# Optimization experiments

Measured on AMD Instinct MI355X. Metric: run time of the kernel, lower is better.

The kernel has to match this reference:

```python
import jax, jax.numpy as jnp
import numpy as np

D_MODEL = 768
N_HEADS = 4
N_POINTS = 4
PATCH = 16
IMG = 224
HF = IMG // PATCH  # 14
WF = IMG // PATCH  # 14
LQ = HF * WF       # 196 tokens
DH = D_MODEL // N_HEADS  # 192


def setup_inputs() -> dict:
    key = jax.random.key(0)
    ks = jax.random.split(key, 14)
    s = 0.02
    inp = {
        "x": jax.random.normal(ks[0], (4, 16, 3, IMG, IMG), dtype=jnp.float32),
        # patch-embed conv (Conv2d 3->768, k=16, s=16)
        "embed_w": s * jax.random.normal(ks[1], (D_MODEL, 3, PATCH, PATCH), dtype=jnp.float32),
        "embed_b": jnp.zeros((D_MODEL,), dtype=jnp.float32),
        # MSDeformAttn linears (nn.Linear stores W as [out, in]; y = x @ W.T + b)
        "value_w": s * jax.random.normal(ks[2], (D_MODEL, D_MODEL), dtype=jnp.float32),
        "value_b": jnp.zeros((D_MODEL,), dtype=jnp.float32),
        "off_w": s * jax.random.normal(ks[3], (N_HEADS * N_POINTS * 2, D_MODEL), dtype=jnp.float32),
        "off_b": s * jax.random.normal(ks[4], (N_HEADS * N_POINTS * 2,), dtype=jnp.float32),
        "aw_w": s * jax.random.normal(ks[5], (N_HEADS * N_POINTS, D_MODEL), dtype=jnp.float32),
        "aw_b": jnp.zeros((N_HEADS * N_POINTS,), dtype=jnp.float32),
        "outp_w": s * jax.random.normal(ks[6], (D_MODEL, D_MODEL), dtype=jnp.float32),
        "outp_b": jnp.zeros((D_MODEL,), dtype=jnp.float32),
        # final nn.Linear proj
        "proj_w": s * jax.random.normal(ks[7], (D_MODEL, D_MODEL), dtype=jnp.float32),
        "proj_b": jnp.zeros((D_MODEL,), dtype=jnp.float32),
    }
    return inp


def _patch_embed(x, w, b):
    # x: (N,3,H,W); non-overlapping 16x16 patches == Conv2d(3,D,16,16)
    N = x.shape[0]
    xh = x.reshape(N, 3, HF, PATCH, WF, PATCH)
    feat = jnp.einsum('nchpwq,dcpq->nhwd', xh, w) + b  # (N,HF,WF,D)
    return feat.reshape(N, LQ, D_MODEL)


def _ref_points():
    lin = jnp.linspace(0.0, 1.0, HF)
    gy, gx = jnp.meshgrid(lin, lin, indexing='ij')
    return jnp.stack([gx, gy], -1).reshape(LQ, 2)  # (Lq, 2) in [0,1], (x,y)


def _deform_attn_core(value, loc, attn):
    # value: (N, Lq, M, Dh); loc: (N, Lq, M, P, 2) normalized [0,1]; attn: (N, Lq, M, P)
    N = value.shape[0]
    # grid_sample align_corners=False: pixel = (2*loc-1 + 1)*S/2 - 0.5 = loc*S - 0.5
    px = loc[..., 0] * WF - 0.5
    py = loc[..., 1] * HF - 0.5
    x0 = jnp.floor(px).astype(jnp.int32)
    y0 = jnp.floor(py).astype(jnp.int32)
    x1, y1 = x0 + 1, y0 + 1
    wx1 = px - x0.astype(px.dtype)
    wy1 = py - y0.astype(py.dtype)
    wx0, wy0 = 1.0 - wx1, 1.0 - wy1

    valh = value.transpose(0, 2, 1, 3)  # (N, M, HW, Dh)

    def gather(ix, iy):
        valid = (ix >= 0) & (ix < WF) & (iy >= 0) & (iy < HF)  # zeros padding
        idx = jnp.clip(iy, 0, HF - 1) * WF + jnp.clip(ix, 0, WF - 1)
        idxm = idx.transpose(0, 2, 1, 3).reshape(N, N_HEADS, LQ * N_POINTS)
        g = jnp.take_along_axis(valh, idxm[..., None], axis=2)  # (N,M,Lq*P,Dh)
        g = g * valid.transpose(0, 2, 1, 3).reshape(N, N_HEADS, LQ * N_POINTS, 1)
        return g.reshape(N, N_HEADS, LQ, N_POINTS, DH)

    def w4(a, b):  # (N,Lq,M,P) -> (N,M,Lq,P,1)
        return (a * b).transpose(0, 2, 1, 3)[..., None]

    sampled = (w4(wx0, wy0) * gather(x0, y0) + w4(wx1, wy0) * gather(x1, y0)
               + w4(wx0, wy1) * gather(x0, y1) + w4(wx1, wy1) * gather(x1, y1))
    # weighted combine over points
    out = (sampled * attn.transpose(0, 2, 1, 3)[..., None]).sum(3)  # (N,M,Lq,Dh)
    return out.transpose(0, 2, 1, 3).reshape(N, LQ, D_MODEL)


def reference(x, embed_w, embed_b, value_w, value_b, off_w, off_b, aw_w, aw_b,
              outp_w, outp_b, proj_w, proj_b):
    B, T = x.shape[0], x.shape[1]
    N = B * T
    xi = x.reshape(N, 3, IMG, IMG)
    feat = _patch_embed(xi, embed_w, embed_b)  # (N, Lq, D)

    # MSDeformAttn (n_levels=1)
    value = (feat @ value_w.T + value_b).reshape(N, LQ, N_HEADS, DH)
    off = (feat @ off_w.T + off_b).reshape(N, LQ, N_HEADS, N_POINTS, 2)
    aw = (feat @ aw_w.T + aw_b).reshape(N, LQ, N_HEADS, N_POINTS)
    aw = jax.nn.softmax(aw, axis=-1)  # softmax over n_levels*n_points = 4

    ref = _ref_points()  # (Lq, 2)
    norm = jnp.array([WF, HF], dtype=feat.dtype)  # offset_normalizer = (W, H)
    loc = ref[None, :, None, None, :] + off / norm  # (N,Lq,M,P,2)

    out = _deform_attn_core(value, loc, aw)
    out = out @ outp_w.T + outp_b  # output_proj

    pooled = out.mean(axis=1)  # mean over tokens
    final = pooled @ proj_w.T + proj_b
    return final.reshape(B, T, D_MODEL)
```

## Files before the change

### kernel.cpp

```cpp
#include <hip/hip_runtime.h>
#include <hip/hip_bf16.h>


using bf16 = __bf16;
typedef bf16  bf16x8 __attribute__((ext_vector_type(8)));
typedef float f32x4  __attribute__((ext_vector_type(4)));

#define N_IMG   64
#define LQ      196
#define DM      768
#define NH      4
#define DH      192
#define M_ROWS  (N_IMG * LQ)
#define NCAT    896

#define B_WGEMM   0
#define B_BCAT    42
#define B_ZERO    46
#define B_IM2COL  94
#define STAGE_GRID (B_IM2COL + 9408)

#define OFF_A     ((size_t)0)
#define OFF_WC    (OFF_A    + 19267584)
#define OFF_BCAT  (OFF_WC   + 1376256)
#define OFF_VBUF  (OFF_BCAT + 4096)
#define OFF_OA    (OFF_VBUF + 19267584)
#define OFF_CORE  (OFF_OA   + 3211264)
#define OFF_POOL  (OFF_CORE + 196608)

__device__ __forceinline__ void gload_lds16(const bf16* g, bf16* l) {
#if __has_builtin(__builtin_amdgcn_global_load_lds)
  __builtin_amdgcn_global_load_lds(
      (const __attribute__((address_space(1))) void*)g,
      (__attribute__((address_space(3))) void*)l, 16, 0, 0);
#else
  *(bf16x8*)l = *(const bf16x8*)g;
#endif
}

__global__ void stage_kernel(const float* __restrict__ x,
                             const float* __restrict__ embed_w,
                             const float* __restrict__ embed_b,
                             const float* __restrict__ value_w,
                             const float* __restrict__ off_w,
                             const float* __restrict__ aw_w,
                             const float* __restrict__ value_b,
                             const float* __restrict__ off_b,
                             const float* __restrict__ aw_b,
                             bf16* __restrict__ A,
                             bf16* __restrict__ Wc,
                             float* __restrict__ bcat2,
                             float* __restrict__ core) {
  __shared__ bf16 As[128 * 64];
  __shared__ bf16 Bs[128 * 64];
  const int bid = blockIdx.x;
  const int tid = threadIdx.x;

  if (bid >= B_IM2COL) {
    const int t   = (bid - B_IM2COL) * 256 + tid;
    const int row = t / 192;
    const int j   = t - row * 192;
    const int k   = j * 4;
    const int c   = k >> 8;
    const int r   = k & 255;
    const int p   = r >> 4;
    const int q   = r & 15;
    const int n   = row / 196;
    const int lq  = row - n * 196;
    const int h   = lq / 14;
    const int w   = lq - h * 14;
    const float4 v = *(const float4*)(x +
        ((((size_t)n * 3 + c) * 224) + h * 16 + p) * 224 + w * 16 + q);
    bf16* dst = A + (size_t)row * DM + k;
    dst[0] = (bf16)v.x; dst[1] = (bf16)v.y; dst[2] = (bf16)v.z; dst[3] = (bf16)v.w;
    return;
  }

  if (bid < B_BCAT) {
    const int mT = bid / 6;
    const int nT = bid - mT * 6;
    const int oBase = mT * 128;
    const int nBase = nT * 128;
    const int wave = tid >> 6;
    const int lane = tid & 63;
    const int quad = lane >> 4;
    const int r16  = lane & 15;
    const int wm = wave & 1;
    const int wn = wave >> 1;
    const int srow = wave * 32 + (lane >> 3);
    const int scol = (lane & 7) * 8;

    const float* asrc[4];
#pragma unroll
    for (int i = 0; i < 4; ++i) {
      const int o = oBase + srow + i * 8;
      asrc[i] = (o < 768) ? value_w + (size_t)o * DM
              : (o < 800) ? off_w + (size_t)(o - 768) * DM
              : (o < 816) ? aw_w + (size_t)(o - 800) * DM : nullptr;
    }

    const f32x4 zero = {0.f, 0.f, 0.f, 0.f};
    f32x4 acc[4][4];
#pragma unroll
    for (int mi = 0; mi < 4; ++mi)
#pragma unroll
      for (int ni = 0; ni < 4; ++ni) acc[mi][ni] = zero;

    for (int kt = 0; kt < DM; kt += 64) {
#pragma unroll
      for (int i = 0; i < 4; ++i) {
        const int r = srow + i * 8;
        bf16x8 av;
        if (asrc[i]) {
          const float4 f0 = *(const float4*)(asrc[i] + kt + scol);
          const float4 f1 = *(const float4*)(asrc[i] + kt + scol + 4);
          av[0] = (bf16)f0.x; av[1] = (bf16)f0.y;
          av[2] = (bf16)f0.z; av[3] = (bf16)f0.w;
          av[4] = (bf16)f1.x; av[5] = (bf16)f1.y;
          av[6] = (bf16)f1.z; av[7] = (bf16)f1.w;
        } else {
#pragma unroll
          for (int jj = 0; jj < 8; ++jj) av[jj] = (bf16)0.f;
        }
        *(bf16x8*)&As[r * 64 + scol] = av;
        const int n = nBase + r;
        bf16x8 bv;
#pragma unroll
        for (int jj = 0; jj < 8; ++jj)
          bv[jj] = (bf16)embed_w[(size_t)(kt + scol + jj) * DM + n];
        *(bf16x8*)&Bs[r * 64 + scol] = bv;
      }
      __syncthreads();
#pragma unroll
      for (int kk = 0; kk < 64; kk += 32) {
        bf16x8 af[4], bfr[4];
#pragma unroll
        for (int mi = 0; mi < 4; ++mi)
          af[mi] = *(const bf16x8*)&As[(wm * 64 + mi * 16 + r16) * 64 + kk + quad * 8];
#pragma unroll
        for (int ni = 0; ni < 4; ++ni)
          bfr[ni] = *(const bf16x8*)&Bs[(wn * 64 + ni * 16 + r16) * 64 + kk + quad * 8];
#pragma unroll
        for (int mi = 0; mi < 4; ++mi)
#pragma unroll
          for (int ni = 0; ni < 4; ++ni)
            acc[mi][ni] = __builtin_amdgcn_mfma_f32_16x16x32_bf16(
                af[mi], bfr[ni], acc[mi][ni], 0, 0, 0);
      }
      __syncthreads();
    }
#pragma unroll
    for (int ni = 0; ni < 4; ++ni) {
      const int col = nBase + wn * 64 + ni * 16 + r16;
#pragma unroll
      for (int mi = 0; mi < 4; ++mi) {
        const int row0 = oBase + wm * 64 + mi * 16 + quad * 4;
#pragma unroll
        for (int rr = 0; rr < 4; ++rr)
          Wc[(size_t)(row0 + rr) * DM + col] = (bf16)acc[mi][ni][rr];
      }
    }
    return;
  }

  if (bid < B_ZERO) {
    const int o = (bid - B_BCAT) * 256 + tid;
    if (o < NCAT) {
      float bias_o = (o < 768) ? value_b[o]
                   : (o < 800) ? off_b[o - 768]
                   : (o < 816) ? aw_b[o - 800] : 0.f;
      float acc = 0.f;
      if (o < 816) {
        const float* wr = (o < 768) ? value_w + (size_t)o * DM
                        : (o < 800) ? off_w + (size_t)(o - 768) * DM
                        : aw_w + (size_t)(o - 800) * DM;
        const float4* w4p = (const float4*)wr;
        const float4* b4p = (const float4*)embed_b;
#pragma unroll 4
        for (int k = 0; k < DM / 4; ++k) {
          const float4 wv = w4p[k], bv = b4p[k];
          acc += wv.x * bv.x + wv.y * bv.y + wv.z * bv.z + wv.w * bv.w;
        }
      }
      bcat2[o] = acc + bias_o;
    }
    return;
  }

  const int i = (bid - B_ZERO) * 256 + tid;
  f32x4 z = {0.f, 0.f, 0.f, 0.f};
  ((f32x4*)core)[i] = z;
}

__global__ void gemm2_mixed(const bf16* __restrict__ A, const bf16* __restrict__ B,
                            const float* __restrict__ bias,
                            bf16* __restrict__ Vb, float* __restrict__ OA,
                            int M, int N, int K) {
  __shared__ bf16 As[128 * 64];
  __shared__ bf16 Bs[128 * 64];

  const int tid  = threadIdx.x;
  const int wave = tid >> 6;
  const int lane = tid & 63;
  const int nBase = blockIdx.x * 128;
  const int mBase = blockIdx.y * 128;
  const int wm = wave & 1;
  const int wn = wave >> 1;
  const int quad = lane >> 4;
  const int r16  = lane & 15;

  const f32x4 zero = {0.f, 0.f, 0.f, 0.f};
  f32x4 acc[4][4];
#pragma unroll
  for (int mi = 0; mi < 4; ++mi)
#pragma unroll
    for (int ni = 0; ni < 4; ++ni) acc[mi][ni] = zero;

  const int srow = wave * 32 + (lane >> 3);
  const int scol = (lane & 7) * 8;
  const bf16* Ag = A + (size_t)(mBase + srow) * K + scol;
  const bf16* Bg = B + (size_t)(nBase + srow) * K + scol;
  bf16* Al = As + srow * 64 + scol;
  bf16* Bl = Bs + srow * 64 + scol;

  for (int kt = 0; kt < K; kt += 64) {
#pragma unroll
    for (int i = 0; i < 4; ++i) {
      gload_lds16(Ag + (size_t)(i * 8) * K + kt, Al + i * 8 * 64);
      gload_lds16(Bg + (size_t)(i * 8) * K + kt, Bl + i * 8 * 64);
    }
    __syncthreads();
#pragma unroll
    for (int kk = 0; kk < 64; kk += 32) {
      bf16x8 af[4], bfr[4];
#pragma unroll
      for (int mi = 0; mi < 4; ++mi)
        af[mi] = *(const bf16x8*)&As[(wm * 64 + mi * 16 + r16) * 64 + kk + quad * 8];
#pragma unroll
      for (int ni = 0; ni < 4; ++ni)
        bfr[ni] = *(const bf16x8*)&Bs[(wn * 64 + ni * 16 + r16) * 64 + kk + quad * 8];
#pragma unroll
      for (int mi = 0; mi < 4; ++mi)
#pragma unroll
        for (int ni = 0; ni < 4; ++ni)
          acc[mi][ni] = __builtin_amdgcn_mfma_f32_16x16x32_bf16(
              af[mi], bfr[ni], acc[mi][ni], 0, 0, 0);
    }
    __syncthreads();
  }

#pragma unroll
  for (int ni = 0; ni < 4; ++ni) {
    const int col = nBase + wn * 64 + ni * 16 + r16;
    const float bv = bias[col];
#pragma unroll
    for (int mi = 0; mi < 4; ++mi) {
      const int row0 = mBase + wm * 64 + mi * 16 + quad * 4;
#pragma unroll
      for (int rr = 0; rr < 4; ++rr) {
        float v = acc[mi][ni][rr] + bv;
        int row = row0 + rr;
        if (col < 768) {
          Vb[(size_t)row * 768 + col] = (bf16)v;
        } else if (col < 816) {
          OA[(size_t)row * 64 + (col - 768)] = v;
        }
      }
    }
  }
}

__global__ void deform_kernel(const bf16* __restrict__ Vb,
                              const float* __restrict__ OA,
                              float* __restrict__ core) {
  __shared__ float s_w[64][4];
  __shared__ int   s_t[64][4];

  const int n   = blockIdx.x;
  const int lq0 = blockIdx.y * 4;
  const int z   = blockIdx.z;
  const int tid = threadIdx.x;

  if (tid < 64) {
    const int i = tid >> 4;
    const int m = (tid >> 2) & 3;
    const int p = tid & 3;
    const int lq = lq0 + i;
    const float* row = OA + ((size_t)n * LQ + lq) * 64;

    const float l0 = row[32 + m * 4 + 0];
    const float l1 = row[32 + m * 4 + 1];
    const float l2 = row[32 + m * 4 + 2];
    const float l3 = row[32 + m * 4 + 3];
    const float mx = fmaxf(fmaxf(l0, l1), fmaxf(l2, l3));
    const float e0 = __expf(l0 - mx), e1 = __expf(l1 - mx);
    const float e2 = __expf(l2 - mx), e3 = __expf(l3 - mx);
    const float inv = 1.f / (e0 + e1 + e2 + e3);
    const float ep[4] = {e0, e1, e2, e3};
    const float ew = ep[p] * inv;

    const int h = lq / 14, w = lq - (lq / 14) * 14;
    const float px = (float)w * (14.f / 13.f) - 0.5f + row[(m * 4 + p) * 2 + 0];
    const float py = (float)h * (14.f / 13.f) - 0.5f + row[(m * 4 + p) * 2 + 1];
    const float fx = floorf(px), fy = floorf(py);
    const int x0 = (int)fx, y0 = (int)fy;
    const float wx1 = px - fx, wy1 = py - fy;
    const float wx0 = 1.f - wx1, wy0 = 1.f - wy1;

    const bool vx0 = (x0 >= 0) & (x0 < 14);
    const bool vx1 = (x0 >= -1) & (x0 < 13);
    const bool vy0 = (y0 >= 0) & (y0 < 14);
    const bool vy1 = (y0 >= -1) & (y0 < 13);
    const int cx0 = min(max(x0, 0), 13),      cx1 = min(max(x0 + 1, 0), 13);
    const int cy0 = min(max(y0, 0), 13) * 14, cy1 = min(max(y0 + 1, 0), 13) * 14;

    s_w[tid][0] = (vx0 & vy0) ? ew * wx0 * wy0 : 0.f;
    s_w[tid][1] = (vx1 & vy0) ? ew * wx1 * wy0 : 0.f;
    s_w[tid][2] = (vx0 & vy1) ? ew * wx0 * wy1 : 0.f;
    s_w[tid][3] = (vx1 & vy1) ? ew * wx1 * wy1 : 0.f;
    s_t[tid][0] = cy0 + cx0;
    s_t[tid][1] = cy0 + cx1;
    s_t[tid][2] = cy1 + cx0;
    s_t[tid][3] = cy1 + cx1;
  }
  __syncthreads();

  const int ch = z * 256 + tid;
  const int m  = ch / DH;
  const bf16* vb = Vb + (size_t)n * LQ * 768 + ch;
  float acc = 0.f;
#pragma unroll
  for (int i = 0; i < 4; ++i) {
#pragma unroll
    for (int p = 0; p < 4; ++p) {
      const int e = i * 16 + m * 4 + p;
      const float4 w4 = *(const float4*)s_w[e];
      const int4   t4 = *(const int4*)s_t[e];
      acc += w4.x * (float)vb[(size_t)t4.x * 768];
      acc += w4.y * (float)vb[(size_t)t4.y * 768];
      acc += w4.z * (float)vb[(size_t)t4.z * 768];
      acc += w4.w * (float)vb[(size_t)t4.w * 768];
    }
  }
  atomicAdd(&core[(size_t)n * DM + ch], acc * (1.f / 196.f));
}

__global__ void small_linear4(const float* __restrict__ in,
                              const float* __restrict__ W,
                              const float* __restrict__ b,
                              float* __restrict__ out) {
  __shared__ float s_in[4 * DM];
  const int tid = threadIdx.x;
  const int n0 = blockIdx.x * 4;
  const float4* src = (const float4*)(in + (size_t)n0 * DM);
#pragma unroll
  for (int i = 0; i < 3; ++i)
    ((float4*)s_in)[tid + i * 256] = src[tid + i * 256];
  __syncthreads();

  const int d = blockIdx.y * 256 + tid;
  const float4* w4p = (const float4*)(W + (size_t)d * DM);
  const float4* s0 = (const float4*)(s_in);
  const float4* s1 = (const float4*)(s_in + DM);
  const float4* s2 = (const float4*)(s_in + 2 * DM);
  const float4* s3 = (const float4*)(s_in + 3 * DM);
  float a0 = 0.f, a1 = 0.f, a2 = 0.f, a3 = 0.f;
#pragma unroll 4
  for (int k = 0; k < DM / 4; ++k) {
    const float4 w = w4p[k];
    const float4 v0 = s0[k], v1 = s1[k], v2 = s2[k], v3 = s3[k];
    a0 += w.x * v0.x + w.y * v0.y + w.z * v0.z + w.w * v0.w;
    a1 += w.x * v1.x + w.y * v1.y + w.z * v1.z + w.w * v1.w;
    a2 += w.x * v2.x + w.y * v2.y + w.z * v2.z + w.w * v2.w;
    a3 += w.x * v3.x + w.y * v3.y + w.z * v3.z + w.w * v3.w;
  }
  const float bv = b[d];
  out[(size_t)(n0 + 0) * DM + d] = a0 + bv;
  out[(size_t)(n0 + 1) * DM + d] = a1 + bv;
  out[(size_t)(n0 + 2) * DM + d] = a2 + bv;
  out[(size_t)(n0 + 3) * DM + d] = a3 + bv;
}

extern "C" void kernel_launch(void* const* d_in, const int* in_sizes, int n_in,
                              void* d_out, int out_size, void* d_ws, size_t ws_size,
                              hipStream_t stream) {
  const float* x       = (const float*)d_in[0];
  const float* embed_w = (const float*)d_in[1];
  const float* embed_b = (const float*)d_in[2];
  const float* value_w = (const float*)d_in[3];
  const float* value_b = (const float*)d_in[4];
  const float* off_w   = (const float*)d_in[5];
  const float* off_b   = (const float*)d_in[6];
  const float* aw_w    = (const float*)d_in[7];
  const float* aw_b    = (const float*)d_in[8];
  const float* outp_w  = (const float*)d_in[9];
  const float* outp_b  = (const float*)d_in[10];
  const float* proj_w  = (const float*)d_in[11];
  const float* proj_b  = (const float*)d_in[12];
  float* out = (float*)d_out;

  char* ws = (char*)d_ws;
  bf16*  A      = (bf16*)(ws + OFF_A);
  bf16*  Wc     = (bf16*)(ws + OFF_WC);
  float* bcat2  = (float*)(ws + OFF_BCAT);
  bf16*  Vbuf   = (bf16*)(ws + OFF_VBUF);
  float* OA     = (float*)(ws + OFF_OA);
  float* core   = (float*)(ws + OFF_CORE);
  float* pooled = (float*)(ws + OFF_POOL);

  stage_kernel<<<dim3(STAGE_GRID), dim3(256), 0, stream>>>(
      x, embed_w, embed_b, value_w, off_w, aw_w, value_b, off_b, aw_b,
      A, Wc, bcat2, core);

  gemm2_mixed<<<dim3(NCAT / 128, M_ROWS / 128), dim3(256), 0, stream>>>(
      A, Wc, bcat2, Vbuf, OA, M_ROWS, NCAT, DM);

  deform_kernel<<<dim3(N_IMG, 49, 3), dim3(256), 0, stream>>>(Vbuf, OA, core);

  small_linear4<<<dim3(N_IMG / 4, 3), dim3(256), 0, stream>>>(core, outp_w, outp_b, pooled);
  small_linear4<<<dim3(N_IMG / 4, 3), dim3(256), 0, stream>>>(pooled, proj_w, proj_b, out);
}
```

Baseline: 279.7 us.

## Split weight prep into separate kernel with pre-transposed bf16 weights for fold GEMM

A new prep kernel converts the concatenated value/offset/attention weights to bf16 and writes a transposed bf16 copy of the patch-embed weight. The weight-folding GEMM then reads these directly from global memory into MFMA fragments, without LDS staging or the strided fp32 loads it did before. The im2col store is also vectorised to 4-wide bf16 writes. This adds a kernel launch and extra workspace traffic in exchange for a cheaper fold GEMM that no longer holds up the long stage kernel.

Result: slower. 287.7 us (+2.9%).

```diff
diff --git a/kernel.cpp b/kernel.cpp
--- a/kernel.cpp
+++ b/kernel.cpp
@@ -3,6 +3,7 @@
 
 
 using bf16 = __bf16;
+typedef bf16  bf16x4 __attribute__((ext_vector_type(4)));
 typedef bf16  bf16x8 __attribute__((ext_vector_type(8)));
 typedef float f32x4  __attribute__((ext_vector_type(4)));
 
@@ -14,19 +15,25 @@
 #define M_ROWS  (N_IMG * LQ)
 #define NCAT    896
 
+#define P_WET    0
+#define P_WCAT   288
+#define P_BCAT   624
+#define P_ZERO   628
+#define PREP_GRID 676
+
 #define B_WGEMM   0
-#define B_BCAT    42
-#define B_ZERO    46
-#define B_IM2COL  94
+#define B_IM2COL  42
 #define STAGE_GRID (B_IM2COL + 9408)
 
 #define OFF_A     ((size_t)0)
-#define OFF_WC    (OFF_A    + 19267584)
-#define OFF_BCAT  (OFF_WC   + 1376256)
-#define OFF_VBUF  (OFF_BCAT + 4096)
-#define OFF_OA    (OFF_VBUF + 19267584)
-#define OFF_CORE  (OFF_OA   + 3211264)
-#define OFF_POOL  (OFF_CORE + 196608)
+#define OFF_WC    (OFF_A     + 19267584)
+#define OFF_BCAT  (OFF_WC    + 1376256)
+#define OFF_VBUF  (OFF_BCAT  + 4096)
+#define OFF_OA    (OFF_VBUF  + 19267584)
+#define OFF_CORE  (OFF_OA    + 3211264)
+#define OFF_POOL  (OFF_CORE  + 196608)
+#define OFF_WCATB (OFF_POOL  + 196608)
+#define OFF_WET   (OFF_WCATB + 1376256)
 
 __device__ __forceinline__ void gload_lds16(const bf16* g, bf16* l) {
 #if __has_builtin(__builtin_amdgcn_global_load_lds)
@@ -38,133 +45,56 @@
 #endif
 }
 
-__global__ void stage_kernel(const float* __restrict__ x,
-                             const float* __restrict__ embed_w,
-                             const float* __restrict__ embed_b,
-                             const float* __restrict__ value_w,
-                             const float* __restrict__ off_w,
-                             const float* __restrict__ aw_w,
-                             const float* __restrict__ value_b,
-                             const float* __restrict__ off_b,
-                             const float* __restrict__ aw_b,
-                             bf16* __restrict__ A,
-                             bf16* __restrict__ Wc,
-                             float* __restrict__ bcat2,
-                             float* __restrict__ core) {
-  __shared__ bf16 As[128 * 64];
-  __shared__ bf16 Bs[128 * 64];
+__global__ void prep_kernel(const float* __restrict__ embed_w,
+                            const float* __restrict__ embed_b,
+                            const float* __restrict__ value_w,
+                            const float* __restrict__ off_w,
+                            const float* __restrict__ aw_w,
+                            const float* __restrict__ value_b,
+                            const float* __restrict__ off_b,
+                            const float* __restrict__ aw_b,
+                            bf16* __restrict__ WeT,
+                            bf16* __restrict__ Wcatb,
+                            float* __restrict__ bcat2,
+                            float* __restrict__ core) {
   const int bid = blockIdx.x;
   const int tid = threadIdx.x;
 
-  if (bid >= B_IM2COL) {
-    const int t   = (bid - B_IM2COL) * 256 + tid;
-    const int row = t / 192;
-    const int j   = t - row * 192;
-    const int k   = j * 4;
-    const int c   = k >> 8;
-    const int r   = k & 255;
-    const int p   = r >> 4;
-    const int q   = r & 15;
-    const int n   = row / 196;
-    const int lq  = row - n * 196;
-    const int h   = lq / 14;
-    const int w   = lq - h * 14;
-    const float4 v = *(const float4*)(x +
-        ((((size_t)n * 3 + c) * 224) + h * 16 + p) * 224 + w * 16 + q);
-    bf16* dst = A + (size_t)row * DM + k;
-    dst[0] = (bf16)v.x; dst[1] = (bf16)v.y; dst[2] = (bf16)v.z; dst[3] = (bf16)v.w;
+  if (bid < P_WCAT) {
+    const int t = bid * 256 + tid;
+    const int e = t / 96;
+    const int g = t - e * 96;
+    bf16x8 o;
+#pragma unroll
+    for (int j = 0; j < 8; ++j)
+      o[j] = (bf16)embed_w[(size_t)(g * 8 + j) * DM + e];
+    *(bf16x8*)(WeT + (size_t)e * DM + g * 8) = o;
     return;
   }
 
-  if (bid < B_BCAT) {
-    const int mT = bid / 6;
-    const int nT = bid - mT * 6;
-    const int oBase = mT * 128;
-    const int nBase = nT * 128;
-    const int wave = tid >> 6;
-    const int lane = tid & 63;
-    const int quad = lane >> 4;
-    const int r16  = lane & 15;
-    const int wm = wave & 1;
-    const int wn = wave >> 1;
-    const int srow = wave * 32 + (lane >> 3);
-    const int scol = (lane & 7) * 8;
-
-    const float* asrc[4];
-#pragma unroll
-    for (int i = 0; i < 4; ++i) {
-      const int o = oBase + srow + i * 8;
-      asrc[i] = (o < 768) ? value_w + (size_t)o * DM
-              : (o < 800) ? off_w + (size_t)(o - 768) * DM
-              : (o < 816) ? aw_w + (size_t)(o - 800) * DM : nullptr;
-    }
-
-    const f32x4 zero = {0.f, 0.f, 0.f, 0.f};
-    f32x4 acc[4][4];
-#pragma unroll
-    for (int mi = 0; mi < 4; ++mi)
-#pragma unroll
-      for (int ni = 0; ni < 4; ++ni) acc[mi][ni] = zero;
-
-    for (int kt = 0; kt < DM; kt += 64) {
-#pragma unroll
-      for (int i = 0; i < 4; ++i) {
-        const int r = srow + i * 8;
-        bf16x8 av;
-        if (asrc[i]) {
-          const float4 f0 = *(const float4*)(asrc[i] + kt + scol);
-          const float4 f1 = *(const float4*)(asrc[i] + kt + scol + 4);
-          av[0] = (bf16)f0.x; av[1] = (bf16)f0.y;
-          av[2] = (bf16)f0.z; av[3] = (bf16)f0.w;
-          av[4] = (bf16)f1.x; av[5] = (bf16)f1.y;
-          av[6] = (bf16)f1.z; av[7] = (bf16)f1.w;
-        } else {
-#pragma unroll
-          for (int jj = 0; jj < 8; ++jj) av[jj] = (bf16)0.f;
-        }
-        *(bf16x8*)&As[r * 64 + scol] = av;
-        const int n = nBase + r;
-        bf16x8 bv;
-#pragma unroll
-        for (int jj = 0; jj < 8; ++jj)
-          bv[jj] = (bf16)embed_w[(size_t)(kt + scol + jj) * DM + n];
-        *(bf16x8*)&Bs[r * 64 + scol] = bv;
-      }
-      __syncthreads();
-#pragma unroll
-      for (int kk = 0; kk < 64; kk += 32) {
-        bf16x8 af[4], bfr[4];
-#pragma unroll
-        for (int mi = 0; mi < 4; ++mi)
-          af[mi] = *(const bf16x8*)&As[(wm * 64 + mi * 16 + r16) * 64 + kk + quad * 8];
-#pragma unroll
-        for (int ni = 0; ni < 4; ++ni)
-          bfr[ni] = *(const bf16x8*)&Bs[(wn * 64 + ni * 16 + r16) * 64 + kk + quad * 8];
-#pragma unroll
-        for (int mi = 0; mi < 4; ++mi)
-#pragma unroll
-          for (int ni = 0; ni < 4; ++ni)
-            acc[mi][ni] = __builtin_amdgcn_mfma_f32_16x16x32_bf16(
-                af[mi], bfr[ni], acc[mi][ni], 0, 0, 0);
-      }
-      __syncthreads();
-    }
-#pragma unroll
-    for (int ni = 0; ni < 4; ++ni) {
-      const int col = nBase + wn * 64 + ni * 16 + r16;
-#pragma unroll
-      for (int mi = 0; mi < 4; ++mi) {
-        const int row0 = oBase + wm * 64 + mi * 16 + quad * 4;
-#pragma unroll
-        for (int rr = 0; rr < 4; ++rr)
-          Wc[(size_t)(row0 + rr) * DM + col] = (bf16)acc[mi][ni][rr];
-      }
-    }
+  if (bid < P_BCAT) {
+    const int t = (bid - P_WCAT) * 256 + tid;
+    const int rr = t / 96;
+    const int g  = t - rr * 96;
+    const float* src = (rr < 768) ? value_w + (size_t)rr * DM
+                     : (rr < 800) ? off_w + (size_t)(rr - 768) * DM
+                     : (rr < 816) ? aw_w + (size_t)(rr - 800) * DM : nullptr;
+    bf16x8 o;
+    if (src) {
+      const float4 f0 = *(const float4*)(src + g * 8);
+      const float4 f1 = *(const float4*)(src + g * 8 + 4);
+      o[0] = (bf16)f0.x; o[1] = (bf16)f0.y; o[2] = (bf16)f0.z; o[3] = (bf16)f0.w;
+      o[4] = (bf16)f1.x; o[5] = (bf16)f1.y; o[6] = (bf16)f1.z; o[7] = (bf16)f1.w;
+    } else {
+#pragma unroll
+      for (int j = 0; j < 8; ++j) o[j] = (bf16)0.f;
+    }
+    *(bf16x8*)(Wcatb + (size_t)rr * DM + g * 8) = o;
     return;
   }
 
-  if (bid < B_ZERO) {
-    const int o = (bid - B_BCAT) * 256 + tid;
+  if (bid < P_ZERO) {
+    const int o = (bid - P_BCAT) * 256 + tid;
     if (o < NCAT) {
       float bias_o = (o < 768) ? value_b[o]
                    : (o < 800) ? off_b[o - 768]
@@ -187,9 +117,89 @@
     return;
   }
 
-  const int i = (bid - B_ZERO) * 256 + tid;
+  const int i = (bid - P_ZERO) * 256 + tid;
   f32x4 z = {0.f, 0.f, 0.f, 0.f};
   ((f32x4*)core)[i] = z;
+}
+
+__global__ void stage_kernel(const float* __restrict__ x,
+                             const bf16* __restrict__ Wcatb,
+                             const bf16* __restrict__ WeT,
+                             bf16* __restrict__ A,
+                             bf16* __restrict__ Wc) {
+  const int bid = blockIdx.x;
+  const int tid = threadIdx.x;
+
+  if (bid >= B_IM2COL) {
+    const int t   = (bid - B_IM2COL) * 256 + tid;
+    const int row = t / 192;
+    const int j   = t - row * 192;
+    const int k   = j * 4;
+    const int c   = k >> 8;
+    const int r   = k & 255;
+    const int p   = r >> 4;
+    const int q   = r & 15;
+    const int n   = row / 196;
+    const int lq  = row - n * 196;
+    const int h   = lq / 14;
+    const int w   = lq - h * 14;
+    const float4 v = *(const float4*)(x +
+        ((((size_t)n * 3 + c) * 224) + h * 16 + p) * 224 + w * 16 + q);
+    bf16x4 o;
+    o[0] = (bf16)v.x; o[1] = (bf16)v.y; o[2] = (bf16)v.z; o[3] = (bf16)v.w;
+    *(bf16x4*)(A + (size_t)row * DM + k) = o;
+    return;
+  }
+
+  const int mT = bid / 6;
+  const int nT = bid - mT * 6;
+  const int oBase = mT * 128;
+  const int eBase = nT * 128;
+  const int wave = tid >> 6;
+  const int lane = tid & 63;
+  const int quad = lane >> 4;
+  const int r16  = lane & 15;
+  const int wm = wave & 1;
+  const int wn = wave >> 1;
+
+  const f32x4 zero = {0.f, 0.f, 0.f, 0.f};
+  f32x4 acc[4][4];
+#pragma unroll
+  for (int mi = 0; mi < 4; ++mi)
+#pragma unroll
+    for (int ni = 0; ni < 4; ++ni) acc[mi][ni] = zero;
+
+  const bf16* Ab = Wcatb + (size_t)(oBase + wm * 64 + r16) * DM + quad * 8;
+  const bf16* Bb = WeT   + (size_t)(eBase + wn * 64 + r16) * DM + quad * 8;
+
+#pragma unroll 2
+  for (int kk = 0; kk < DM; kk += 32) {
+    bf16x8 af[4], bfr[4];
+#pragma unroll
+    for (int mi = 0; mi < 4; ++mi)
+      af[mi] = *(const bf16x8*)(Ab + (size_t)mi * 16 * DM + kk);
+#pragma unroll
+    for (int ni = 0; ni < 4; ++ni)
+      bfr[ni] = *(const bf16x8*)(Bb + (size_t)ni * 16 * DM + kk);
+#pragma unroll
+    for (int mi = 0; mi < 4; ++mi)
+#pragma unroll
+      for (int ni = 0; ni < 4; ++ni)
+        acc[mi][ni] = __builtin_amdgcn_mfma_f32_16x16x32_bf16(
+            af[mi], bfr[ni], acc[mi][ni], 0, 0, 0);
+  }
+
+#pragma unroll
+  for (int ni = 0; ni < 4; ++ni) {
+    const int col = eBase + wn * 64 + ni * 16 + r16;
+#pragma unroll
+    for (int mi = 0; mi < 4; ++mi) {
+      const int row0 = oBase + wm * 64 + mi * 16 + quad * 4;
+#pragma unroll
+      for (int rr = 0; rr < 4; ++rr)
+        Wc[(size_t)(row0 + rr) * DM + col] = (bf16)acc[mi][ni][rr];
+    }
+  }
 }
 
 __global__ void gemm2_mixed(const bf16* __restrict__ A, const bf16* __restrict__ B,
@@ -407,10 +417,15 @@
   float* OA     = (float*)(ws + OFF_OA);
   float* core   = (float*)(ws + OFF_CORE);
   float* pooled = (float*)(ws + OFF_POOL);
+  bf16*  Wcatb  = (bf16*)(ws + OFF_WCATB);
+  bf16*  WeT    = (bf16*)(ws + OFF_WET);
+
+  prep_kernel<<<dim3(PREP_GRID), dim3(256), 0, stream>>>(
+      embed_w, embed_b, value_w, off_w, aw_w, value_b, off_b, aw_b,
+      WeT, Wcatb, bcat2, core);
 
   stage_kernel<<<dim3(STAGE_GRID), dim3(256), 0, stream>>>(
-      x, embed_w, embed_b, value_w, off_w, aw_w, value_b, off_b, aw_b,
-      A, Wc, bcat2, core);
+      x, Wcatb, WeT, A, Wc);
 
   gemm2_mixed<<<dim3(NCAT / 128, M_ROWS / 128), dim3(256), 0, stream>>>(
       A, Wc, bcat2, Vbuf, OA, M_ROWS, NCAT, DM);
```
